# Kernel tuning notes

Hardware: AMD Instinct MI355X
Metric: run time of the kernel (lower is better)

The kernel has to match this reference:

```python
import jax, jax.numpy as jnp
import numpy as np

SPARSITY_RATIO = 0.1


def setup_inputs() -> dict:
    key = jax.random.key(0)
    x = jax.random.normal(key, (4, 4096, 2048), dtype=jnp.float32)
    return {"x": x}


def reference(x):
    # x: [batch, seq_len, n_embd]
    B, S, D = x.shape
    k = max(1, int(D * SPARSITY_RATIO))
    # top-k by absolute value along the feature dim
    _, topk_idx = jax.lax.top_k(jnp.abs(x), k)  # [B, S, k]
    # scatter 1.0 at top-k positions (matches torch scatter_ mask construction)
    b = jnp.arange(B)[:, None, None]
    s = jnp.arange(S)[None, :, None]
    mask = jnp.zeros_like(x).at[b, s, topk_idx].set(1.0)
    scale = jnp.asarray(D / k, dtype=x.dtype)
    return x * mask * scale
```

## Files before the change

### kernel.cpp

```cpp
#include <hip/hip_runtime.h>


constexpr int D_DIM = 2048;
constexpr int K_SEL = 204;
constexpr int NT    = 256;
constexpr int RPW   = 2;

typedef float f32x4 __attribute__((ext_vector_type(4)));

__device__ __forceinline__ int dpp_reduce_add(int x) {
    x += __builtin_amdgcn_update_dpp(0, x, 0x111, 0xF, 0xF, true);
    x += __builtin_amdgcn_update_dpp(0, x, 0x112, 0xF, 0xF, true);
    x += __builtin_amdgcn_update_dpp(0, x, 0x114, 0xF, 0xF, true);
    x += __builtin_amdgcn_update_dpp(0, x, 0x118, 0xF, 0xF, true);
    x += __builtin_amdgcn_update_dpp(0, x, 0x142, 0xA, 0xF, false);
    x += __builtin_amdgcn_update_dpp(0, x, 0x143, 0xC, 0xF, false);
    return __builtin_amdgcn_readlane(x, 63);
}

__device__ __forceinline__ int wave_count_ge(const float4 (&f)[8], float t) {
    int c0 = 0, c1 = 0, c2 = 0, c3 = 0;
#pragma unroll
    for (int b = 0; b < 8; ++b) {
        c0 += (__builtin_fabsf(f[b].x) >= t) ? 1 : 0;
        c1 += (__builtin_fabsf(f[b].y) >= t) ? 1 : 0;
        c2 += (__builtin_fabsf(f[b].z) >= t) ? 1 : 0;
        c3 += (__builtin_fabsf(f[b].w) >= t) ? 1 : 0;
    }
    return dpp_reduce_add((c0 + c1) + (c2 + c3));
}

__device__ __forceinline__ void process_row(const float4 (&f)[8],
                                            float* __restrict__ outr,
                                            const int lane) {
    const float scale = 2048.0f / 204.0f;

    unsigned lo = 0u, hi = 0x80000000u;
    unsigned thr = 0u;
    bool done = false;

    {
        const int c = wave_count_ge(f, 1.6484375f);
        if (c == K_SEL) { thr = 0x3FD30000u; done = true; }
        else if (c > K_SEL) lo = 0x3FD30000u; else hi = 0x3FD30000u;
    }
    if (!done) {
        const unsigned p2 = (lo != 0u) ? 0x3FD60000u
                                       : 0x3FD00000u;
        const int c = wave_count_ge(f, __uint_as_float(p2));
        if (c == K_SEL) { thr = p2; done = true; }
        else if (c > K_SEL) lo = p2; else hi = p2;
    }
    if (!done) {
        unsigned p3 = 0u;
        if (hi == 0x80000000u)      p3 = 0x3FE00000u;
        else if (lo == 0u)          p3 = 0x3FC80000u;
        if (p3 != 0u) {
            const int c = wave_count_ge(f, __uint_as_float(p3));
            if (c == K_SEL) { thr = p3; done = true; }
            else if (c > K_SEL) lo = p3; else hi = p3;
        }
    }
    if (!done && lo == 0u) {
        const int c = wave_count_ge(f, 1.0f);
        if (c == K_SEL) { thr = 0x3F800000u; done = true; }
        else if (c > K_SEL) lo = 0x3F800000u; else hi = 0x3F800000u;
    }

#pragma unroll 1
    while (!done && (hi - lo) > 1u) {
        const unsigned mid = (lo + hi) >> 1;
        const int c = wave_count_ge(f, __uint_as_float(mid));
        if (c == K_SEL) { thr = mid; done = true; }
        else if (c > K_SEL) lo = mid; else hi = mid;
    }

    f32x4* op = reinterpret_cast<f32x4*>(outr);

    if (done) {
        const float tf = __uint_as_float(thr);
#pragma unroll
        for (int b = 0; b < 8; ++b) {
            f32x4 w;
            w.x = (__builtin_fabsf(f[b].x) >= tf) ? f[b].x * scale : 0.0f;
            w.y = (__builtin_fabsf(f[b].y) >= tf) ? f[b].y * scale : 0.0f;
            w.z = (__builtin_fabsf(f[b].z) >= tf) ? f[b].z * scale : 0.0f;
            w.w = (__builtin_fabsf(f[b].w) >= tf) ? f[b].w * scale : 0.0f;
            __builtin_nontemporal_store(w, op + b * 64 + lane);
        }
        return;
    }

    const float Tf = __uint_as_float(lo);
    int ge_pack = 0;
#pragma unroll
    for (int b = 0; b < 8; ++b) {
        ge_pack += (__builtin_fabsf(f[b].x) > Tf) ? 1 : 0;
        ge_pack += (__builtin_fabsf(f[b].y) > Tf) ? 1 : 0;
        ge_pack += (__builtin_fabsf(f[b].z) > Tf) ? 1 : 0;
        ge_pack += (__builtin_fabsf(f[b].w) > Tf) ? 1 : 0;
        ge_pack += (__builtin_fabsf(f[b].x) == Tf) ? (1 << 16) : 0;
        ge_pack += (__builtin_fabsf(f[b].y) == Tf) ? (1 << 16) : 0;
        ge_pack += (__builtin_fabsf(f[b].z) == Tf) ? (1 << 16) : 0;
        ge_pack += (__builtin_fabsf(f[b].w) == Tf) ? (1 << 16) : 0;
    }
    const int tot = dpp_reduce_add(ge_pack);
    const int cnt_gt = tot & 0xFFFF;
    const int neq = tot >> 16;
    const int r = K_SEL - cnt_gt;

    if (neq == r) {
#pragma unroll
        for (int b = 0; b < 8; ++b) {
            f32x4 w;
            w.x = (__builtin_fabsf(f[b].x) >= Tf) ? f[b].x * scale : 0.0f;
            w.y = (__builtin_fabsf(f[b].y) >= Tf) ? f[b].y * scale : 0.0f;
            w.z = (__builtin_fabsf(f[b].z) >= Tf) ? f[b].z * scale : 0.0f;
            w.w = (__builtin_fabsf(f[b].w) >= Tf) ? f[b].w * scale : 0.0f;
            __builtin_nontemporal_store(w, op + b * 64 + lane);
        }
        return;
    }

    const unsigned long long lt = (lane == 0) ? 0ull : (~0ull >> (64 - lane));
    int base = 0;
    for (int b = 0; b < 8; ++b) {
        const float fe[4] = { f[b].x, f[b].y, f[b].z, f[b].w };
        unsigned long long m[4];
#pragma unroll
        for (int e = 0; e < 4; ++e) m[e] = __ballot(__builtin_fabsf(fe[e]) == Tf);
        int cm = 0;
#pragma unroll
        for (int e = 0; e < 4; ++e) cm += __popcll(m[e] & lt);
        f32x4 w;
        float wv[4];
        int partial = 0;
#pragma unroll
        for (int e = 0; e < 4; ++e) {
            const int rank = base + cm + partial;
            const bool eq = (__builtin_fabsf(fe[e]) == Tf);
            const bool sel = (__builtin_fabsf(fe[e]) > Tf) || (eq && rank < r);
            wv[e] = sel ? fe[e] * scale : 0.0f;
            partial += (int)((m[e] >> lane) & 1ull);
        }
        w.x = wv[0]; w.y = wv[1]; w.z = wv[2]; w.w = wv[3];
        __builtin_nontemporal_store(w, op + b * 64 + lane);
#pragma unroll
        for (int e = 0; e < 4; ++e) base += __popcll(m[e]);
    }
}

__global__ __launch_bounds__(NT) void sparse_topk_kernel(const float* __restrict__ x,
                                                         float* __restrict__ out) {
    const int wave = threadIdx.x >> 6;
    const int lane = threadIdx.x & 63;
    const long long gw = (long long)blockIdx.x * 4 + wave;
    const long long r0 = gw * RPW;

    const float4* xp0 = reinterpret_cast<const float4*>(x + r0 * D_DIM);
    const float4* xp1 = reinterpret_cast<const float4*>(x + (r0 + 1) * D_DIM);

    float4 fA[8], fB[8];
#pragma unroll
    for (int b = 0; b < 8; ++b) fA[b] = xp0[b * 64 + lane];
#pragma unroll
    for (int b = 0; b < 8; ++b) fB[b] = xp1[b * 64 + lane];

    process_row(fA, out + r0 * D_DIM, lane);
    process_row(fB, out + (r0 + 1) * D_DIM, lane);
}

extern "C" void kernel_launch(void* const* d_in, const int* in_sizes, int n_in,
                              void* d_out, int out_size, void* d_ws, size_t ws_size,
                              hipStream_t stream) {
    const float* x = (const float*)d_in[0];
    float* out = (float*)d_out;
    const int rows = in_sizes[0] / D_DIM;
    sparse_topk_kernel<<<rows / (4 * RPW), NT, 0, stream>>>(x, out);
}
```

Baseline: 242.2 us.

## Software-pipeline row loads across threshold search with manual vmcnt waits

Each wave now handles four rows instead of two. While the binary-search probes for the current row run, the kernel issues the global loads for a later row through inline-asm dwordx4 loads, spread one per probe step behind scheduling barriers. Explicit s_waitcnt vmcnt waits rotate three register buffers so load latency overlaps the compare-and-reduce work. The cost is higher register pressure (three 8xf32x4 buffers, with launch bounds raised to 2 blocks), half as many blocks, and wait counts that depend on the exact order in which loads and stores are issued.

```diff
diff --git a/kernel.cpp b/kernel.cpp
--- a/kernel.cpp
+++ b/kernel.cpp
@@ -4,9 +4,21 @@
 constexpr int D_DIM = 2048;
 constexpr int K_SEL = 204;
 constexpr int NT    = 256;
-constexpr int RPW   = 2;
+constexpr int RPW   = 4;
 
 typedef float f32x4 __attribute__((ext_vector_type(4)));
+
+__device__ __forceinline__ void gload16(f32x4& dst, const f32x4* p) {
+    asm volatile("global_load_dwordx4 %0, %1, off" : "=v"(dst) : "v"(p) : "memory");
+}
+
+#define VMWAIT(n)                                                  \
+    do {                                                           \
+        asm volatile("s_waitcnt vmcnt(" #n ")" ::: "memory");      \
+        __builtin_amdgcn_sched_barrier(0);                         \
+    } while (0)
+
+#define SCHED_FENCE() __builtin_amdgcn_sched_barrier(0)
 
 __device__ __forceinline__ int dpp_reduce_add(int x) {
     x += __builtin_amdgcn_update_dpp(0, x, 0x111, 0xF, 0xF, true);
@@ -18,7 +30,7 @@
     return __builtin_amdgcn_readlane(x, 63);
 }
 
-__device__ __forceinline__ int wave_count_ge(const float4 (&f)[8], float t) {
+__device__ __forceinline__ int wave_count_ge(const f32x4 (&f)[8], float t) {
     int c0 = 0, c1 = 0, c2 = 0, c3 = 0;
 #pragma unroll
     for (int b = 0; b < 8; ++b) {
@@ -30,52 +42,62 @@
     return dpp_reduce_add((c0 + c1) + (c2 + c3));
 }
 
-__device__ __forceinline__ void process_row(const float4 (&f)[8],
-                                            float* __restrict__ outr,
-                                            const int lane) {
+__device__ __forceinline__ void probe_step(const f32x4 (&f)[8], unsigned t,
+                                           unsigned& lo, unsigned& hi,
+                                           unsigned& thr, bool& done) {
+    const int c = wave_count_ge(f, __uint_as_float(t));
+    if (c == K_SEL) { thr = t; done = true; }
+    else if (c > K_SEL) lo = t; else hi = t;
+}
+
+template <bool PF>
+__device__ __forceinline__ void process_row(const f32x4 (&f)[8],
+                                            f32x4 (&nbuf)[8],
+                                            const f32x4* psrc,
+                                            f32x4* op, const int lane) {
     const float scale = 2048.0f / 204.0f;
 
     unsigned lo = 0u, hi = 0x80000000u;
     unsigned thr = 0u;
     bool done = false;
 
-    {
-        const int c = wave_count_ge(f, 1.6484375f);
-        if (c == K_SEL) { thr = 0x3FD30000u; done = true; }
-        else if (c > K_SEL) lo = 0x3FD30000u; else hi = 0x3FD30000u;
-    }
-    if (!done) {
-        const unsigned p2 = (lo != 0u) ? 0x3FD60000u
-                                       : 0x3FD00000u;
-        const int c = wave_count_ge(f, __uint_as_float(p2));
-        if (c == K_SEL) { thr = p2; done = true; }
-        else if (c > K_SEL) lo = p2; else hi = p2;
-    }
+    if (PF) gload16(nbuf[0], psrc + 0 * 64 + lane);
+    probe_step(f, 0x3FD30000u, lo, hi, thr, done);
+    SCHED_FENCE();
+
+    if (PF) gload16(nbuf[1], psrc + 1 * 64 + lane);
+    if (!done)
+        probe_step(f, (lo != 0u) ? 0x3FD60000u : 0x3FD00000u,
+                   lo, hi, thr, done);
+    SCHED_FENCE();
+
+    if (PF) gload16(nbuf[2], psrc + 2 * 64 + lane);
     if (!done) {
         unsigned p3 = 0u;
         if (hi == 0x80000000u)      p3 = 0x3FE00000u;
         else if (lo == 0u)          p3 = 0x3FC80000u;
-        if (p3 != 0u) {
-            const int c = wave_count_ge(f, __uint_as_float(p3));
-            if (c == K_SEL) { thr = p3; done = true; }
-            else if (c > K_SEL) lo = p3; else hi = p3;
-        }
-    }
-    if (!done && lo == 0u) {
-        const int c = wave_count_ge(f, 1.0f);
-        if (c == K_SEL) { thr = 0x3F800000u; done = true; }
-        else if (c > K_SEL) lo = 0x3F800000u; else hi = 0x3F800000u;
+        if (p3 != 0u) probe_step(f, p3, lo, hi, thr, done);
+    }
+    SCHED_FENCE();
+
+    if (PF) gload16(nbuf[3], psrc + 3 * 64 + lane);
+    if (!done) {
+        if (lo == 0u)               probe_step(f, 0x3F800000u, lo, hi, thr, done);
+        else if ((hi - lo) > 1u)    probe_step(f, (lo + hi) >> 1, lo, hi, thr, done);
+    }
+    SCHED_FENCE();
+
+#pragma unroll
+    for (int s = 4; s < 8; ++s) {
+        if (PF) gload16(nbuf[s], psrc + s * 64 + lane);
+        if (!done && (hi - lo) > 1u)
+            probe_step(f, (lo + hi) >> 1, lo, hi, thr, done);
+        SCHED_FENCE();
     }
 
 #pragma unroll 1
-    while (!done && (hi - lo) > 1u) {
-        const unsigned mid = (lo + hi) >> 1;
-        const int c = wave_count_ge(f, __uint_as_float(mid));
-        if (c == K_SEL) { thr = mid; done = true; }
-        else if (c > K_SEL) lo = mid; else hi = mid;
-    }
-
-    f32x4* op = reinterpret_cast<f32x4*>(outr);
+    while (!done && (hi - lo) > 1u)
+        probe_step(f, (lo + hi) >> 1, lo, hi, thr, done);
 
     if (done) {
         const float tf = __uint_as_float(thr);
@@ -150,24 +172,27 @@
     }
 }
 
-__global__ __launch_bounds__(NT) void sparse_topk_kernel(const float* __restrict__ x,
-                                                         float* __restrict__ out) {
+__global__ __launch_bounds__(NT, 2) void sparse_topk_kernel(
+        const float* __restrict__ x, float* __restrict__ out) {
     const int wave = threadIdx.x >> 6;
     const int lane = threadIdx.x & 63;
     const long long gw = (long long)blockIdx.x * 4 + wave;
     const long long r0 = gw * RPW;
 
-    const float4* xp0 = reinterpret_cast<const float4*>(x + r0 * D_DIM);
-    const float4* xp1 = reinterpret_cast<const float4*>(x + (r0 + 1) * D_DIM);
-
-    float4 fA[8], fB[8];
-#pragma unroll
-    for (int b = 0; b < 8; ++b) fA[b] = xp0[b * 64 + lane];
-#pragma unroll
-    for (int b = 0; b < 8; ++b) fB[b] = xp1[b * 64 + lane];
-
-    process_row(fA, out + r0 * D_DIM, lane);
-    process_row(fB, out + (r0 + 1) * D_DIM, lane);
+    const f32x4* xw = reinterpret_cast<const f32x4*>(x + r0 * D_DIM);
+    f32x4* ow = reinterpret_cast<f32x4*>(out + r0 * D_DIM);
+
+    f32x4 A[8], B[8], C[8];
+
+#pragma unroll
+    for (int b = 0; b < 8; ++b) gload16(A[b], xw + b * 64 + lane);
+#pragma unroll
+    for (int b = 0; b < 8; ++b) gload16(B[b], xw + 512 + b * 64 + lane);
+
+    VMWAIT(8); process_row<true >(A, C, xw + 1024, ow,            lane);
+    VMWAIT(8); process_row<true >(B, A, xw + 1536, ow + 512,      lane);
+    VMWAIT(8); process_row<false>(C, B, xw,        ow + 1024,     lane);
+    VMWAIT(0); process_row<false>(A, B, xw,        ow + 1536,     lane);
 }
 
 extern "C" void kernel_launch(void* const* d_in, const int* in_sizes, int n_in,
```

Result: faster. 237.4 us (-2.0%).
